# Kernel optimization log

Hardware: AMD Instinct MI355X
Metric: run time of the kernel (lower is better)

The kernel has to match this reference:

```python
import jax, jax.numpy as jnp
import numpy as np
from jax import lax

B, N, H, W, C = 8, 1024, 256, 256, 256
HID = 512
RATES = (1, 3, 9, 9, 3, 1)


def setup_inputs() -> dict:
    key = jax.random.key(0)
    ks = jax.random.split(key, 16)
    # vertices are (row, col) float coordinates inside the feature map
    vertices = jax.random.uniform(ks[0], (B, N, 2), jnp.float32) * jnp.array([H - 1, W - 1], jnp.float32)
    features = jax.random.normal(ks[1], (B, H, W, C), jnp.float32)
    inp = {"vertices": vertices, "features": features}
    # Conv1D stack params (haiku Conv1D: kernel [K, Cin, Cout], bias [Cout])
    cin = C
    for i in range(6):
        inp[f"w{i}"] = jax.random.normal(ks[2 + 2 * i], (3, cin, HID), jnp.float32) * 0.05
        inp[f"b{i}"] = jax.random.normal(ks[3 + 2 * i], (HID,), jnp.float32) * 0.05
        cin = HID
    # offset head: Conv1D(2, 1, with_bias=False); original zero-init, randomized here
    inp["w_off"] = jax.random.normal(ks[14], (1, HID, 2), jnp.float32) * 0.05
    return inp


def _conv1d(x, w, b, rate):
    # x: [B, N, Cin], w: [K, Cin, Cout] -> SAME-padded dilated conv over vertex axis
    y = lax.conv_general_dilated(x, w, window_strides=(1,), padding="SAME",
                                 rhs_dilation=(rate,),
                                 dimension_numbers=("NWC", "WIO", "NWC"))
    return y if b is None else y + b


def _sample_at_vertices(vertices, features):
    # bilinear interpolation, zero outside (map_coordinates order=1 mode='constant')
    Bb, Hh, Ww, Cc = features.shape
    y, x = vertices[..., 0], vertices[..., 1]  # [B, N]
    y0f, x0f = jnp.floor(y), jnp.floor(x)
    wy1, wx1 = y - y0f, x - x0f
    wy0, wx0 = 1.0 - wy1, 1.0 - wx1
    y0, x0 = y0f.astype(jnp.int32), x0f.astype(jnp.int32)
    flat = features.reshape(Bb, Hh * Ww, Cc)

    def gather(yi, xi, wgt):
        valid = (yi >= 0) & (yi < Hh) & (xi >= 0) & (xi < Ww)
        idx = jnp.clip(yi, 0, Hh - 1) * Ww + jnp.clip(xi, 0, Ww - 1)  # [B, N]
        vals = jnp.take_along_axis(flat, idx[..., None], axis=1)  # [B, N, C]
        return vals * (wgt * valid)[..., None]

    return (gather(y0, x0, wy0 * wx0) + gather(y0, x0 + 1, wy0 * wx1)
            + gather(y0 + 1, x0, wy1 * wx0) + gather(y0 + 1, x0 + 1, wy1 * wx1))


def reference(vertices, features, w0, b0, w1, b1, w2, b2, w3, b3, w4, b4, w5, b5, w_off):
    h = _sample_at_vertices(vertices, features)  # [B, N, C]
    ws = (w0, w1, w2, w3, w4, w5)
    bs = (b0, b1, b2, b3, b4, b5)
    for w, b, r in zip(ws, bs, RATES):
        h = jax.nn.relu(_conv1d(h, w, b, r))
    offsets = _conv1d(h, w_off, None, 1)  # [B, N, 2]
    return vertices + offsets
```

## Files before the change

kernel.cpp:

```cpp
#include <hip/hip_runtime.h>

#define BATCH 8
#define NPTS  1024
#define FH    256
#define FW    256
#define FC    256
#define HID   512
#define PADN  1056
#define HALO  16

typedef __attribute__((ext_vector_type(8))) short short8;
typedef __attribute__((ext_vector_type(16))) float f32x16;
typedef unsigned short ushort_t;
typedef unsigned int uint_t;

__device__ __forceinline__ ushort_t f2bf(float f) {
    uint_t u = __builtin_bit_cast(uint_t, f);
    u += 0x7fffu + ((u >> 16) & 1u);
    return (ushort_t)(u >> 16);
}
__device__ __forceinline__ float bf2f(ushort_t s) {
    uint_t u = ((uint_t)s) << 16;
    return __builtin_bit_cast(float, u);
}

#define GLOAD16(g, l)                                                     \
    __builtin_amdgcn_global_load_lds(                                     \
        (const __attribute__((address_space(1))) void*)(g),               \
        (__attribute__((address_space(3))) void*)(l), 16, 0, 0)

__global__ __launch_bounds__(256) void prep_kernel(
    const float* __restrict__ vertices, const float* __restrict__ features,
    const float* __restrict__ w0, const float* __restrict__ w1,
    const float* __restrict__ w2, const float* __restrict__ w3,
    const float* __restrict__ w4, const float* __restrict__ w5,
    ushort_t* __restrict__ wt0, ushort_t* __restrict__ wt1,
    ushort_t* __restrict__ wt2, ushort_t* __restrict__ wt3,
    ushort_t* __restrict__ wt4, ushort_t* __restrict__ wt5,
    ushort_t* __restrict__ XpA, ushort_t* __restrict__ XpB,
    ushort_t* __restrict__ XpC)
{
    __shared__ float tile[64][65];
    const int blk = blockIdx.x;
    const int tid = threadIdx.x;

    if (blk < 1280) {
        int i = blk * 256 + tid;
        if (i < 65536) {
            int b = i >> 13, rem = i & 8191;
            int strip = rem >> 12, off = rem & 4095;
            XpA[(size_t)b * (PADN * FC) + (strip ? (PADN - HALO) * FC : 0) + off] = 0;
        }
        int jB = i - 65536;
        if (jB >= 0 && jB < 262144) {
            ushort_t* T = (jB < 131072) ? XpB : XpC;
            int j = jB & 131071;
            int b = j >> 14, rem = j & 16383;
            int strip = rem >> 13, off = rem & 8191;
            T[(size_t)b * (PADN * HID) + (strip ? (PADN - HALO) * HID : 0) + off] = 0;
        }
        return;
    }

    if (blk < 2336) {
        int j = blk - 1280;
        const float* w; ushort_t* wt; int CIN, kk0, co0;
        if (j < 96) {
            w = w0; wt = wt0; CIN = FC;
            kk0 = (j % 12) * 64; co0 = (j / 12) * 64;
        } else {
            int j2 = j - 96;
            int layer = j2 / 192, jj = j2 % 192;
            const float* ws[5]  = {w1, w2, w3, w4, w5};
            ushort_t*   wts[5]  = {wt1, wt2, wt3, wt4, wt5};
            w = ws[layer]; wt = wts[layer]; CIN = HID;
            kk0 = (jj % 24) * 64; co0 = (jj / 24) * 64;
        }
        int tap = kk0 / CIN, ci0 = kk0 - tap * CIN;
        int K3 = 3 * CIN;
#pragma unroll 4
        for (int it = 0; it < 16; ++it) {
            int r = it * 4 + (tid >> 6);
            tile[r][tid & 63] = w[((size_t)tap * CIN + ci0 + r) * HID + co0 + (tid & 63)];
        }
        __syncthreads();
#pragma unroll 4
        for (int it = 0; it < 16; ++it) {
            int co = it * 4 + (tid >> 6);
            wt[(size_t)(co0 + co) * K3 + kk0 + (tid & 63)] = f2bf(tile[tid & 63][co]);
        }
        return;
    }

    {
        int p = (blk - 2336) * 4 + (tid >> 6);
        int b = p >> 10;
        int n = p & 1023;
        int t = tid & 63;

        float y = vertices[2 * p + 0];
        float x = vertices[2 * p + 1];
        float y0f = floorf(y), x0f = floorf(x);
        float wy1 = y - y0f, wx1 = x - x0f;
        float wy0 = 1.f - wy1, wx0 = 1.f - wx1;
        int y0 = (int)y0f, x0 = (int)x0f;

        float4 acc = make_float4(0.f, 0.f, 0.f, 0.f);
        const float4* fbase = (const float4*)features + (size_t)b * FH * FW * (FC / 4);

#define CORNER(yi, xi, wgt) {                                                  \
        int yy = (yi), xx = (xi);                                              \
        float wv = ((yy >= 0) && (yy < FH) && (xx >= 0) && (xx < FW)) ? (wgt) : 0.f; \
        int yc = yy < 0 ? 0 : (yy > FH - 1 ? FH - 1 : yy);                     \
        int xc = xx < 0 ? 0 : (xx > FW - 1 ? FW - 1 : xx);                     \
        float4 v = fbase[((size_t)yc * FW + xc) * (FC / 4) + t];               \
        acc.x += v.x * wv; acc.y += v.y * wv; acc.z += v.z * wv; acc.w += v.w * wv; }

        CORNER(y0,     x0,     wy0 * wx0);
        CORNER(y0,     x0 + 1, wy0 * wx1);
        CORNER(y0 + 1, x0,     wy1 * wx0);
        CORNER(y0 + 1, x0 + 1, wy1 * wx1);
#undef CORNER

        ushort4 o;
        o.x = f2bf(acc.x); o.y = f2bf(acc.y); o.z = f2bf(acc.z); o.w = f2bf(acc.w);
        *(ushort4*)(XpA + ((size_t)b * PADN + HALO + n) * FC + 4 * t) = o;
    }
}

template <int CIN>
__global__ __launch_bounds__(256) void conv_mfma(
    const ushort_t* __restrict__ Xp,
    const ushort_t* __restrict__ Wt,
    const float* __restrict__ bias,
    ushort_t* __restrict__ Yp,
    int rate)
{
    constexpr int K3 = 3 * CIN;
    constexpr int NT = K3 / 64;
    __shared__ short lds[3][12288];

    const int tid  = threadIdx.x;
    const int wid  = tid >> 6;
    const int lane = tid & 63;
    const int wm   = wid >> 1, wn = wid & 1;

    const int h  = blockIdx.x;
    const int bm = (h & 7) * 8 + (h >> 6);
    const int bn = (h >> 3) & 7;
    const int batch = bm >> 3;
    const int n0    = (bm & 7) * 128;
    const int co0   = bn * 64;

    const short* Xbase = (const short*)Xp + ((size_t)batch * PADN + HALO + n0) * CIN;
    const short* Wbase = (const short*)Wt + (size_t)co0 * K3;

    auto stage = [&](int buf, int kt) {
        const int tap = (kt << 6) / CIN;
        const int ci0 = (kt << 6) - tap * CIN;
        const short* Ag = Xbase + (ptrdiff_t)(tap - 1) * rate * CIN + ci0;
        const short* Bg = Wbase + (kt << 6);
        short* ldsA = &lds[buf][0];
        short* ldsB = &lds[buf][8192];
#pragma unroll
        for (int it = 0; it < 4; ++it) {
            int row  = wid * 32 + it * 8 + (lane >> 3);
            int chnk = (lane & 7) ^ (row & 7);
            GLOAD16(Ag + (size_t)row * CIN + chnk * 8, ldsA + ((wid * 4 + it) << 9));
        }
#pragma unroll
        for (int it = 0; it < 2; ++it) {
            int row  = wid * 16 + it * 8 + (lane >> 3);
            int chnk = (lane & 7) ^ (row & 7);
            GLOAD16(Bg + (size_t)row * K3 + chnk * 8, ldsB + ((wid * 2 + it) << 9));
        }
    };

    f32x16 acc[2];
    const int rowA0 = wm * 64 + (lane & 31);
    const int coB   = wn * 32 + (lane & 31);
    {
        float bv = bias[co0 + coB];
#pragma unroll
        for (int i = 0; i < 2; ++i)
#pragma unroll
            for (int r = 0; r < 16; ++r) acc[i][r] = bv;
    }

    stage(0, 0);
    stage(1, 1);

    int cur = 0;
    for (int kt = 0; kt < NT; ++kt) {
        if (kt + 1 < NT) {
            asm volatile("s_waitcnt vmcnt(6)" ::: "memory");
        } else {
            asm volatile("s_waitcnt vmcnt(0)" ::: "memory");
        }
        __builtin_amdgcn_s_barrier();
        __builtin_amdgcn_sched_barrier(0);

        if (kt + 2 < NT) {
            int nb = cur + 2; if (nb >= 3) nb -= 3;
            stage(nb, kt + 2);
        }

        const short* As = &lds[cur][0];
        const short* Bs = &lds[cur][8192];
        __builtin_amdgcn_s_setprio(1);
#pragma unroll
        for (int ks = 0; ks < 4; ++ks) {
            int ch = ks * 2 + (lane >> 5);
            short8 av[2], bv;
#pragma unroll
            for (int i = 0; i < 2; ++i) {
                int ra = rowA0 + i * 32;
                av[i] = *(const short8*)(As + ra * 64 + ((ch ^ (ra & 7)) << 3));
            }
            bv = *(const short8*)(Bs + coB * 64 + ((ch ^ (coB & 7)) << 3));
#pragma unroll
            for (int i = 0; i < 2; ++i)
                acc[i] = __builtin_amdgcn_mfma_f32_32x32x16_bf16(
                    av[i], bv, acc[i], 0, 0, 0);
        }
        __builtin_amdgcn_s_setprio(0);
        cur += 1; if (cur >= 3) cur -= 3;
    }

    ushort_t* Yb = Yp + ((size_t)batch * PADN + HALO + n0) * HID + co0;
#pragma unroll
    for (int i = 0; i < 2; ++i) {
#pragma unroll
        for (int r = 0; r < 16; ++r) {
            int rrow = wm * 64 + i * 32 + (r & 3) + 8 * (r >> 2) + 4 * (lane >> 5);
            float v = acc[i][r];
            v = v > 0.f ? v : 0.f;
            Yb[(size_t)rrow * HID + coB] = f2bf(v);
        }
    }
}

__global__ __launch_bounds__(64) void head_kernel(
    const ushort_t* __restrict__ h, const float* __restrict__ w_off,
    const float* __restrict__ vertices, float* __restrict__ out)
{
    int p = blockIdx.x;
    int b = p >> 10, n = p & 1023;
    int t = threadIdx.x;
    const ushort_t* hr = h + ((size_t)b * PADN + HALO + n) * HID + t * 8;

    uint4 raw = *(const uint4*)hr;
    ushort_t hv[8];
    hv[0] = raw.x & 0xffff; hv[1] = raw.x >> 16;
    hv[2] = raw.y & 0xffff; hv[3] = raw.y >> 16;
    hv[4] = raw.z & 0xffff; hv[5] = raw.z >> 16;
    hv[6] = raw.w & 0xffff; hv[7] = raw.w >> 16;

    float s0 = 0.f, s1 = 0.f;
#pragma unroll
    for (int k = 0; k < 8; ++k) {
        float x = bf2f(hv[k]);
        s0 += x * w_off[(t * 8 + k) * 2 + 0];
        s1 += x * w_off[(t * 8 + k) * 2 + 1];
    }
#pragma unroll
    for (int off = 32; off >= 1; off >>= 1) {
        s0 += __shfl_down(s0, off);
        s1 += __shfl_down(s1, off);
    }
    if (t == 0) {
        out[2 * p + 0] = vertices[2 * p + 0] + s0;
        out[2 * p + 1] = vertices[2 * p + 1] + s1;
    }
}

extern "C" void kernel_launch(void* const* d_in, const int* in_sizes, int n_in,
                              void* d_out, int out_size, void* d_ws, size_t ws_size,
                              hipStream_t stream)
{
    (void)in_sizes; (void)n_in; (void)out_size; (void)ws_size;

    const float* vertices = (const float*)d_in[0];
    const float* features = (const float*)d_in[1];
    const float* w[6]  = {(const float*)d_in[2], (const float*)d_in[4],
                          (const float*)d_in[6], (const float*)d_in[8],
                          (const float*)d_in[10], (const float*)d_in[12]};
    const float* bb[6] = {(const float*)d_in[3], (const float*)d_in[5],
                          (const float*)d_in[7], (const float*)d_in[9],
                          (const float*)d_in[11], (const float*)d_in[13]};
    const float* w_off = (const float*)d_in[14];
    float* out = (float*)d_out;

    char* p = (char*)d_ws;
    ushort_t* wt[6];
    wt[0] = (ushort_t*)p; p += (size_t)HID * (3 * FC) * 2;
    for (int i = 1; i < 6; ++i) { wt[i] = (ushort_t*)p; p += (size_t)HID * (3 * HID) * 2; }
    ushort_t* XpA = (ushort_t*)p; p += (size_t)BATCH * PADN * FC  * 2;
    ushort_t* XpB = (ushort_t*)p; p += (size_t)BATCH * PADN * HID * 2;
    ushort_t* XpC = (ushort_t*)p;

    prep_kernel<<<4384, 256, 0, stream>>>(
        vertices, features, w[0], w[1], w[2], w[3], w[4], w[5],
        wt[0], wt[1], wt[2], wt[3], wt[4], wt[5], XpA, XpB, XpC);

    static const int rates[6] = {1, 3, 9, 9, 3, 1};
    conv_mfma<FC><<<512, 256, 0, stream>>>(XpA, wt[0], bb[0], XpB, rates[0]);
    ushort_t* src = XpB;
    ushort_t* dst = XpC;
    for (int i = 1; i < 6; ++i) {
        conv_mfma<HID><<<512, 256, 0, stream>>>(src, wt[i], bb[i], dst, rates[i]);
        ushort_t* tmp = src; src = dst; dst = tmp;
    }

    head_kernel<<<BATCH * NPTS, 64, 0, stream>>>(src, w_off, vertices, out);
}
```

Before: 131.3 us.

## Pre-swizzle weights into MFMA fragment layout and load B directly to registers

```diff
diff --git a/kernel.cpp b/kernel.cpp
--- a/kernel.cpp
+++ b/kernel.cpp
@@ -77,17 +77,29 @@
             kk0 = (jj % 24) * 64; co0 = (jj / 24) * 64;
         }
         int tap = kk0 / CIN, ci0 = kk0 - tap * CIN;
-        int K3 = 3 * CIN;
+        int SL  = (3 * CIN) >> 4;
 #pragma unroll 4
         for (int it = 0; it < 16; ++it) {
             int r = it * 4 + (tid >> 6);
             tile[r][tid & 63] = w[((size_t)tap * CIN + ci0 + r) * HID + co0 + (tid & 63)];
         }
         __syncthreads();
-#pragma unroll 4
-        for (int it = 0; it < 16; ++it) {
-            int co = it * 4 + (tid >> 6);
-            wt[(size_t)(co0 + co) * K3 + kk0 + (tid & 63)] = f2bf(tile[tid & 63][co]);
+        int gl  = tid >> 7;
+        int r2  = tid & 127;
+        int l   = r2 >> 1;
+        int j0  = (r2 & 1) * 4;
+        int gco = (co0 >> 5) + gl;
+        int kb  = ((l >> 5) << 3);
+        int cl  = gl * 32 + (l & 31);
+#pragma unroll
+        for (int si = 0; si < 4; ++si) {
+            int s = (kk0 >> 4) + si;
+            ushort4 v;
+            v.x = f2bf(tile[si * 16 + kb + j0 + 0][cl]);
+            v.y = f2bf(tile[si * 16 + kb + j0 + 1][cl]);
+            v.z = f2bf(tile[si * 16 + kb + j0 + 2][cl]);
+            v.w = f2bf(tile[si * 16 + kb + j0 + 3][cl]);
+            *(ushort4*)(wt + ((((size_t)gco * SL) + s) << 9) + l * 8 + j0) = v;
         }
         return;
     }
@@ -131,14 +143,15 @@
 template <int CIN>
 __global__ __launch_bounds__(256) void conv_mfma(
     const ushort_t* __restrict__ Xp,
-    const ushort_t* __restrict__ Wt,
+    const ushort_t* __restrict__ Wf,
     const float* __restrict__ bias,
     ushort_t* __restrict__ Yp,
     int rate)
 {
     constexpr int K3 = 3 * CIN;
     constexpr int NT = K3 / 64;
-    __shared__ short lds[3][12288];
+    constexpr int SL = K3 / 16;
+    __shared__ short lds[3][8192];
 
     const int tid  = threadIdx.x;
     const int wid  = tid >> 6;
@@ -153,27 +166,25 @@
     const int co0   = bn * 64;
 
     const short* Xbase = (const short*)Xp + ((size_t)batch * PADN + HALO + n0) * CIN;
-    const short* Wbase = (const short*)Wt + (size_t)co0 * K3;
-
-    auto stage = [&](int buf, int kt) {
+    const short* Wb = (const short*)Wf
+                    + (((size_t)(bn * 2 + wn) * SL) << 9) + lane * 8;
+
+    auto stageA = [&](int buf, int kt) {
         const int tap = (kt << 6) / CIN;
         const int ci0 = (kt << 6) - tap * CIN;
         const short* Ag = Xbase + (ptrdiff_t)(tap - 1) * rate * CIN + ci0;
-        const short* Bg = Wbase + (kt << 6);
         short* ldsA = &lds[buf][0];
-        short* ldsB = &lds[buf][8192];
 #pragma unroll
         for (int it = 0; it < 4; ++it) {
             int row  = wid * 32 + it * 8 + (lane >> 3);
             int chnk = (lane & 7) ^ (row & 7);
             GLOAD16(Ag + (size_t)row * CIN + chnk * 8, ldsA + ((wid * 4 + it) << 9));
         }
-#pragma unroll
-        for (int it = 0; it < 2; ++it) {
-            int row  = wid * 16 + it * 8 + (lane >> 3);
-            int chnk = (lane & 7) ^ (row & 7);
-            GLOAD16(Bg + (size_t)row * K3 + chnk * 8, ldsB + ((wid * 2 + it) << 9));
-        }
+    };
+    auto loadB = [&](short8* dst, int kt) {
+        const short* p = Wb + ((size_t)(kt * 4) << 9);
+#pragma unroll
+        for (int ks = 0; ks < 4; ++ks) dst[ks] = *(const short8*)(p + (ks << 9));
     };
 
     f32x16 acc[2];
@@ -187,44 +198,48 @@
             for (int r = 0; r < 16; ++r) acc[i][r] = bv;
     }
 
-    stage(0, 0);
-    stage(1, 1);
+    short8 B0[4], B1[4];
+    stageA(0, 0);
+    loadB(B0, 0);
+    stageA(1, 1);
 
     int cur = 0;
-    for (int kt = 0; kt < NT; ++kt) {
-        if (kt + 1 < NT) {
-            asm volatile("s_waitcnt vmcnt(6)" ::: "memory");
-        } else {
-            asm volatile("s_waitcnt vmcnt(0)" ::: "memory");
-        }
+    auto kstep = [&](int s, short8* Bcur, short8* Bnxt) {
+        if (s == NT - 1) asm volatile("s_waitcnt vmcnt(0)" ::: "memory");
+        else             asm volatile("s_waitcnt vmcnt(4)" ::: "memory");
         __builtin_amdgcn_s_barrier();
         __builtin_amdgcn_sched_barrier(0);
 
-        if (kt + 2 < NT) {
+        if (s + 1 < NT) loadB(Bnxt, s + 1);
+        __builtin_amdgcn_sched_barrier(0);
+        if (s + 2 < NT) {
             int nb = cur + 2; if (nb >= 3) nb -= 3;
-            stage(nb, kt + 2);
+            stageA(nb, s + 2);
         }
 
         const short* As = &lds[cur][0];
-        const short* Bs = &lds[cur][8192];
         __builtin_amdgcn_s_setprio(1);
 #pragma unroll
         for (int ks = 0; ks < 4; ++ks) {
             int ch = ks * 2 + (lane >> 5);
-            short8 av[2], bv;
+            short8 av[2];
 #pragma unroll
             for (int i = 0; i < 2; ++i) {
                 int ra = rowA0 + i * 32;
                 av[i] = *(const short8*)(As + ra * 64 + ((ch ^ (ra & 7)) << 3));
             }
-            bv = *(const short8*)(Bs + coB * 64 + ((ch ^ (coB & 7)) << 3));
 #pragma unroll
             for (int i = 0; i < 2; ++i)
                 acc[i] = __builtin_amdgcn_mfma_f32_32x32x16_bf16(
-                    av[i], bv, acc[i], 0, 0, 0);
+                    av[i], Bcur[ks], acc[i], 0, 0, 0);
         }
         __builtin_amdgcn_s_setprio(0);
         cur += 1; if (cur >= 3) cur -= 3;
+    };
+
+    for (int kt = 0; kt < NT; kt += 2) {
+        kstep(kt,     B0, B1);
+        kstep(kt + 1, B1, B0);
     }
 
     ushort_t* Yb = Yp + ((size_t)batch * PADN + HALO + n0) * HID + co0;
```

New measurement: 133.0 us. About the same (+1.3%).
